# Kernel tuning notes

Measured on AMD Instinct MI355X. Metric: run time of the kernel, lower is better.

The kernel has to match this reference:

```python
import jax, jax.numpy as jnp
import numpy as np

N, E = 50000, 400000          # nodes, edges
T, R = 4, 8                   # node types, relations (edge types)
H, DK = 8, 32                 # heads, head dim
DIN = DOUT = 256              # in/out feature dim (DOUT = H*DK)
SQRT_DK = float(np.sqrt(DK))


def setup_inputs() -> dict:
    key = jax.random.key(0)
    ks = jax.random.split(key, 12)
    f32 = jnp.float32
    return {
        "x": jax.random.normal(ks[0], (N, DIN), f32),
        "node_type": jax.random.randint(ks[1], (N,), 0, T, jnp.int32),
        "src": jax.random.randint(ks[2], (E,), 0, N, jnp.int32),
        "dst": jax.random.randint(ks[3], (E,), 0, N, jnp.int32),
        "etype": jax.random.randint(ks[4], (E,), 0, R, jnp.int32),
        "Wk": jax.random.normal(ks[5], (T, DOUT, DIN), f32) / np.sqrt(DIN).astype(np.float32),
        "bk": jnp.zeros((T, DOUT), f32),
        "Wq": jax.random.normal(ks[6], (T, DOUT, DIN), f32) / np.sqrt(DIN).astype(np.float32),
        "bq": jnp.zeros((T, DOUT), f32),
        "Wv": jax.random.normal(ks[7], (T, DOUT, DIN), f32) / np.sqrt(DIN).astype(np.float32),
        "bv": jnp.zeros((T, DOUT), f32),
        "Wa": jax.random.normal(ks[8], (T, DOUT, DOUT), f32) / np.sqrt(DOUT).astype(np.float32),
        "ba": jnp.zeros((T, DOUT), f32),
        "rel_pri": jnp.ones((R, H), f32),
        "rel_att": jax.random.normal(ks[9], (R, H, DK, DK), f32) / np.sqrt(DK).astype(np.float32),  # ~xavier
        "rel_msg": jax.random.normal(ks[10], (R, H, DK, DK), f32) / np.sqrt(DK).astype(np.float32),
        "skip": jnp.ones((T,), f32),
    }


def _typed_linear(h, W, b, ntype):
    # per-node-type linear: y_n = W[type_n] @ h_n + b[type_n]
    y = jnp.einsum('ni,tdi->ntd', h, W)                      # [N,T,D] (T is small)
    y = jnp.take_along_axis(y, ntype[:, None, None], axis=1)[:, 0]
    return y + b[ntype]


def _hgt_forward(x, node_type, src, dst, etype,
                 Wk, bk, Wq, bq, Wv, bv, Wa, ba,
                 rel_pri, rel_att, rel_msg, skip):
    # typed k/q/v projections -> [N,H,DK]
    K = _typed_linear(x, Wk, bk, node_type).reshape(N, H, DK)
    Q = _typed_linear(x, Wq, bq, node_type).reshape(N, H, DK)
    V = _typed_linear(x, Wv, bv, node_type).reshape(N, H, DK)

    k_e, q_e, v_e = K[src], Q[dst], V[src]                   # [E,H,DK] gathers

    # per-relation head transforms (loop over small fixed R, masked accumulate)
    key_e = jnp.zeros_like(k_e)
    msg_e = jnp.zeros_like(v_e)
    for r in range(R):
        m = (etype == r)[:, None, None].astype(x.dtype)
        key_e = key_e + m * jnp.einsum('ehd,hdf->ehf', k_e, rel_att[r])
        msg_e = msg_e + m * jnp.einsum('ehd,hdf->ehf', v_e, rel_msg[r])

    att = (q_e * key_e).sum(-1) * rel_pri[etype] / SQRT_DK   # [E,H]

    # softmax per (dst node, edge type) segment, then mean across edge types
    seg = dst * R + etype                                    # [E]
    S = N * R
    amax = jax.ops.segment_max(att, seg, num_segments=S)     # [S,H]
    ex = jnp.exp(att - amax[seg])
    denom = jax.ops.segment_sum(ex, seg, num_segments=S)
    w = ex / denom[seg]                                      # normalized attention [E,H]
    h_seg = jax.ops.segment_sum(w[:, :, None] * msg_e, seg, num_segments=S)  # [S,H,DK]
    cnt = jax.ops.segment_sum(jnp.ones((E,), x.dtype), seg, num_segments=S)  # [S]

    h_nr = h_seg.reshape(N, R, DOUT)
    present = (cnt.reshape(N, R) > 0).astype(x.dtype)        # which etypes hit each node
    t = h_nr.sum(1) / jnp.maximum(present.sum(1), 1.0)[:, None]  # cross_reducer='mean'

    trans = _typed_linear(t, Wa, ba, node_type)              # per-type output linear
    alpha = jax.nn.sigmoid(skip)[node_type][:, None]
    return trans * alpha + x * (1.0 - alpha)


def reference(x, node_type, src, dst, etype,
              Wk, bk, Wq, bq, Wv, bv, Wa, ba,
              rel_pri, rel_att, rel_msg, skip):
    return _hgt_forward(x, node_type, src, dst, etype,
                        Wk, bk, Wq, bq, Wv, bv, Wa, ba,
                        rel_pri, rel_att, rel_msg, skip)
```

## Files before the change

### kernel.cpp

```cpp
#include <hip/hip_runtime.h>
#include <math.h>
#include <stdint.h>

#define N_NODES 50000
#define N_EDGES 400000
#define N_T 4
#define N_R 8
#define N_H 8
#define DKD 32
#define D 256
#define TM 64
#define N_SEG (N_NODES * N_R)
#define PROJ_BLOCKS ((N_NODES + TM - 1) / TM + N_T)

typedef __bf16 v8bf __attribute__((ext_vector_type(8)));
typedef float v4f __attribute__((ext_vector_type(4)));
typedef unsigned short u16;

__device__ __forceinline__ u16 f2bf(float f) {
    unsigned int u = __float_as_uint(f);
    u += 0x7fffu + ((u >> 16) & 1u);
    return (u16)(u >> 16);
}

__device__ __forceinline__ void load_bf32(const u16* __restrict__ p, float* f) {
    const uint4* p4 = (const uint4*)p;
    #pragma unroll
    for (int j = 0; j < 4; j++) {
        uint4 u = p4[j];
        f[8 * j + 0] = __uint_as_float(u.x << 16);
        f[8 * j + 1] = __uint_as_float(u.x & 0xffff0000u);
        f[8 * j + 2] = __uint_as_float(u.y << 16);
        f[8 * j + 3] = __uint_as_float(u.y & 0xffff0000u);
        f[8 * j + 4] = __uint_as_float(u.z << 16);
        f[8 * j + 5] = __uint_as_float(u.z & 0xffff0000u);
        f[8 * j + 6] = __uint_as_float(u.w << 16);
        f[8 * j + 7] = __uint_as_float(u.w & 0xffff0000u);
    }
}

__device__ __forceinline__ float dot8f(uint4 m, const float* v) {
    float s;
    s  = __uint_as_float(m.x << 16)          * v[0];
    s += __uint_as_float(m.x & 0xffff0000u)  * v[1];
    s += __uint_as_float(m.y << 16)          * v[2];
    s += __uint_as_float(m.y & 0xffff0000u)  * v[3];
    s += __uint_as_float(m.z << 16)          * v[4];
    s += __uint_as_float(m.z & 0xffff0000u)  * v[5];
    s += __uint_as_float(m.w << 16)          * v[6];
    s += __uint_as_float(m.w & 0xffff0000u)  * v[7];
    return s;
}

__global__ __launch_bounds__(256) void k_cvt4(const float4* __restrict__ s,
                                              ushort4* __restrict__ d, int n4) {
    int i = blockIdx.x * 256 + threadIdx.x;
    if (i < n4) {
        float4 v = s[i];
        ushort4 o;
        o.x = f2bf(v.x); o.y = f2bf(v.y); o.z = f2bf(v.z); o.w = f2bf(v.w);
        d[i] = o;
    }
}

__global__ __launch_bounds__(256) void k_cvt_t(const float* __restrict__ s,
                                               u16* __restrict__ d) {
    int i = blockIdx.x * 256 + threadIdx.x;
    if (i >= N_R * N_H * DKD * DKD) return;
    int mat = i >> 10, w = i & 1023;
    int d0 = w >> 5, f = w & 31;
    d[(mat << 10) + f * DKD + d0] = f2bf(s[i]);
}

__global__ void k_hist(const int* __restrict__ nt, int* __restrict__ cnt) {
    int n = blockIdx.x * blockDim.x + threadIdx.x;
    if (n < N_NODES) atomicAdd(&cnt[nt[n]], 1);
}

__global__ void k_scan(const int* __restrict__ cnt, int* __restrict__ off,
                       int* __restrict__ toff) {
    int o = 0, to = 0;
    for (int t = 0; t < N_T; t++) {
        off[t] = o; toff[t] = to;
        o += cnt[t]; to += (cnt[t] + TM - 1) / TM;
    }
    off[N_T] = o; toff[N_T] = to;
}

__global__ void k_scatter(const int* __restrict__ nt, const int* __restrict__ off,
                          int* __restrict__ cur, int* __restrict__ order) {
    int n = blockIdx.x * blockDim.x + threadIdx.x;
    if (n >= N_NODES) return;
    int t = nt[n];
    int pos = off[t] + atomicAdd(&cur[t], 1);
    order[pos] = n;
}

__global__ void k_hist_seg(const int* __restrict__ dst, const int* __restrict__ et,
                           int* __restrict__ cnt) {
    int e = blockIdx.x * blockDim.x + threadIdx.x;
    if (e < N_EDGES) atomicAdd(&cnt[dst[e] * N_R + et[e]], 1);
}

__global__ __launch_bounds__(1024) void k_scan_l1(const int* __restrict__ cnt,
                                                  int* __restrict__ excl,
                                                  int* __restrict__ bsum) {
    __shared__ int sh[1024];
    int tid = threadIdx.x, i = blockIdx.x * 1024 + tid;
    int v = (i < N_SEG) ? cnt[i] : 0;
    sh[tid] = v;
    __syncthreads();
    #pragma unroll
    for (int ofs = 1; ofs < 1024; ofs <<= 1) {
        int t = (tid >= ofs) ? sh[tid - ofs] : 0;
        __syncthreads();
        sh[tid] += t;
        __syncthreads();
    }
    if (i < N_SEG) excl[i] = sh[tid] - v;
    if (tid == 1023) bsum[blockIdx.x] = sh[1023];
}

__global__ __launch_bounds__(512) void k_scan_l2(int* __restrict__ bsum, int NB) {
    __shared__ int sh[512];
    int tid = threadIdx.x;
    int v = (tid < NB) ? bsum[tid] : 0;
    sh[tid] = v;
    __syncthreads();
    #pragma unroll
    for (int ofs = 1; ofs < 512; ofs <<= 1) {
        int t = (tid >= ofs) ? sh[tid - ofs] : 0;
        __syncthreads();
        sh[tid] += t;
        __syncthreads();
    }
    if (tid < NB) bsum[tid] = sh[tid] - v;
}

__global__ void k_scan_l3(int* __restrict__ excl, const int* __restrict__ bsum) {
    int i = blockIdx.x * blockDim.x + threadIdx.x;
    if (i < N_SEG) excl[i] += bsum[i >> 10];
    else if (i == N_SEG) excl[N_SEG] = N_EDGES;
}

__global__ void k_scatter_seg(const int* __restrict__ src, const int* __restrict__ dst,
                              const int* __restrict__ et, const int* __restrict__ rp,
                              int* __restrict__ cur, int* __restrict__ esrc) {
    int e = blockIdx.x * blockDim.x + threadIdx.x;
    if (e >= N_EDGES) return;
    int sg = dst[e] * N_R + et[e];
    int pos = rp[sg] + atomicAdd(&cur[sg], 1);
    esrc[pos] = src[e];
}

__global__ __launch_bounds__(256) void k_proj(
    const float* __restrict__ x, const int* __restrict__ order,
    const int* __restrict__ off, const int* __restrict__ toff,
    const u16* __restrict__ Wkb, const float* __restrict__ bk,
    const u16* __restrict__ Wqb, const float* __restrict__ bq,
    const u16* __restrict__ Wvb, const float* __restrict__ bv,
    u16* __restrict__ Kb, u16* __restrict__ Qb, u16* __restrict__ Vb) {
    __shared__ __align__(16) u16 xs[TM][D + 8];
    int b = blockIdx.x;
    int t = -1;
    #pragma unroll
    for (int i = 0; i < N_T; i++)
        if (b >= toff[i] && b < toff[i + 1]) t = i;
    if (t < 0) return;
    int nodeBase = off[t] + (b - toff[t]) * TM;
    int count = min(TM, off[t + 1] - nodeBase);
    int tid = threadIdx.x;

    for (int j = tid; j < TM * (D / 4); j += 256) {
        int row = j >> 6, ch = j & 63;
        float4 v = {0.f, 0.f, 0.f, 0.f};
        if (row < count) {
            int g = order[nodeBase + row];
            v = *(const float4*)(x + (size_t)g * D + ch * 4);
        }
        ushort4 o;
        o.x = f2bf(v.x); o.y = f2bf(v.y); o.z = f2bf(v.z); o.w = f2bf(v.w);
        *(ushort4*)&xs[row][ch * 4] = o;
    }
    __syncthreads();

    int lane = tid & 63, wave = tid >> 6;
    int m = lane & 15, quad = lane >> 4;
    v8bf a[8];
    #pragma unroll
    for (int ks = 0; ks < 8; ks++)
        a[ks] = *(const v8bf*)&xs[wave * 16 + m][ks * 32 + quad * 8];

    int grow[4]; bool vrow[4];
    #pragma unroll
    for (int r = 0; r < 4; r++) {
        int rowi = wave * 16 + quad * 4 + r;
        vrow[r] = (rowi < count);
        grow[r] = vrow[r] ? order[nodeBase + rowi] : 0;
    }

    const u16* Ws[3] = {Wkb + (size_t)t * D * D, Wqb + (size_t)t * D * D, Wvb + (size_t)t * D * D};
    const float* Bs[3] = {bk + t * D, bq + t * D, bv + t * D};
    u16* Os[3] = {Kb, Qb, Vb};

    for (int p = 0; p < 3; p++) {
        const u16* W = Ws[p];
        for (int dt = 0; dt < 16; dt++) {
            int dcol = dt * 16 + m;
            v4f acc = {0.f, 0.f, 0.f, 0.f};
            #pragma unroll
            for (int ks = 0; ks < 8; ks++) {
                v8bf bf = *(const v8bf*)(W + (size_t)dcol * D + ks * 32 + quad * 8);
                acc = __builtin_amdgcn_mfma_f32_16x16x32_bf16(a[ks], bf, acc, 0, 0, 0);
            }
            float bias = Bs[p][dcol];
            #pragma unroll
            for (int r = 0; r < 4; r++) {
                if (vrow[r])
                    Os[p][(size_t)grow[r] * D + dcol] = f2bf(acc[r] + bias);
            }
        }
    }
}

__global__ __launch_bounds__(256) void k_fused(
    const u16* __restrict__ Kb, u16* QTb, const u16* __restrict__ Vb,
    const int* __restrict__ rowptr, const int* __restrict__ esrc,
    const u16* __restrict__ Ab, const u16* __restrict__ Mtb,
    const float* __restrict__ pri) {
    __shared__ __align__(16) float Uld[4][N_H][40];
    int wave = threadIdx.x >> 6, lane = threadIdx.x & 63;
    int n = blockIdx.x * 4 + wave;
    if (n >= N_NODES) return;
    int h = lane >> 3, fo = (lane & 7) * 4;
    int base = n * N_R;

    float qv[32];
    load_bf32(QTb + (size_t)n * D + h * DKD, qv);

    float macc[4] = {0.f, 0.f, 0.f, 0.f};
    int np = 0;

    #pragma unroll
    for (int r = 0; r < N_R; r++) {
        int s0 = rowptr[base + r], s1 = rowptr[base + r + 1];
        if (s0 >= s1) continue;
        np++;

        const u16* Ar = Ab + ((size_t)(r * N_H + h) * DKD + fo) * DKD;
        float qtv[4];
        #pragma unroll
        for (int i = 0; i < 4; i++) {
            const uint4* ar = (const uint4*)(Ar + i * DKD);
            qtv[i] = dot8f(ar[0], qv) + dot8f(ar[1], qv + 8)
                   + dot8f(ar[2], qv + 16) + dot8f(ar[3], qv + 24);
        }
        float scale = pri[r * N_H + h] * 0.17677669529663687f;

        float dtmp = 0.f, u0 = 0.f, u1 = 0.f, u2 = 0.f, u3 = 0.f;
        for (int ei = s0; ei < s1; ei++) {
            int s = esrc[ei];
            uint2 ku = *(const uint2*)(Kb + (size_t)s * D + h * DKD + fo);
            uint2 vu = *(const uint2*)(Vb + (size_t)s * D + h * DKD + fo);
            float p = __uint_as_float(ku.x << 16)         * qtv[0]
                    + __uint_as_float(ku.x & 0xffff0000u) * qtv[1]
                    + __uint_as_float(ku.y << 16)         * qtv[2]
                    + __uint_as_float(ku.y & 0xffff0000u) * qtv[3];
            p += __shfl_xor(p, 1);
            p += __shfl_xor(p, 2);
            p += __shfl_xor(p, 4);
            float ex = __expf(p * scale);
            dtmp += ex;
            u0 += ex * __uint_as_float(vu.x << 16);
            u1 += ex * __uint_as_float(vu.x & 0xffff0000u);
            u2 += ex * __uint_as_float(vu.y << 16);
            u3 += ex * __uint_as_float(vu.y & 0xffff0000u);
        }

        float invd = 1.f / dtmp;
        float4 uw = {u0 * invd, u1 * invd, u2 * invd, u3 * invd};
        __builtin_amdgcn_wave_barrier();
        *(float4*)&Uld[wave][h][fo] = uw;
        __builtin_amdgcn_wave_barrier();

        float Uv[32];
        #pragma unroll
        for (int i = 0; i < 8; i++)
            *(float4*)&Uv[4 * i] = *(const float4*)&Uld[wave][h][4 * i];

        const u16* mp = Mtb + ((size_t)(r * N_H + h) * DKD + fo) * DKD;
        #pragma unroll
        for (int j = 0; j < 4; j++) {
            const uint4* mr = (const uint4*)(mp + j * DKD);
            macc[j] += dot8f(mr[0], Uv) + dot8f(mr[1], Uv + 8)
                     + dot8f(mr[2], Uv + 16) + dot8f(mr[3], Uv + 24);
        }
        __builtin_amdgcn_wave_barrier();
    }

    float invp = (np > 0) ? 1.f / (float)np : 1.f;
    ushort4 o;
    o.x = f2bf(macc[0] * invp); o.y = f2bf(macc[1] * invp);
    o.z = f2bf(macc[2] * invp); o.w = f2bf(macc[3] * invp);
    *(ushort4*)(QTb + (size_t)n * D + h * DKD + fo) = o;
}

__global__ __launch_bounds__(256) void k_out(
    const u16* __restrict__ TBF, const float* __restrict__ x,
    const int* __restrict__ order, const int* __restrict__ off, const int* __restrict__ toff,
    const u16* __restrict__ Wab, const float* __restrict__ ba,
    const float* __restrict__ skip, float* __restrict__ out) {
    __shared__ __align__(16) u16 xs[TM][D + 8];
    int b = blockIdx.x;
    int t = -1;
    #pragma unroll
    for (int i = 0; i < N_T; i++)
        if (b >= toff[i] && b < toff[i + 1]) t = i;
    if (t < 0) return;
    int nodeBase = off[t] + (b - toff[t]) * TM;
    int count = min(TM, off[t + 1] - nodeBase);
    int tid = threadIdx.x;

    for (int j = tid; j < TM * 32; j += 256) {
        int row = j >> 5, ch = j & 31;
        ushort4 z = {0, 0, 0, 0};
        if (row < count) {
            int g = order[nodeBase + row];
            const ushort4* p = (const ushort4*)(TBF + (size_t)g * D + ch * 8);
            *(ushort4*)&xs[row][ch * 8] = p[0];
            *(ushort4*)&xs[row][ch * 8 + 4] = p[1];
        } else {
            *(ushort4*)&xs[row][ch * 8] = z;
            *(ushort4*)&xs[row][ch * 8 + 4] = z;
        }
    }
    __syncthreads();

    int lane = tid & 63, wave = tid >> 6;
    int m = lane & 15, quad = lane >> 4;
    v8bf a[8];
    #pragma unroll
    for (int ks = 0; ks < 8; ks++)
        a[ks] = *(const v8bf*)&xs[wave * 16 + m][ks * 32 + quad * 8];

    int grow[4]; bool vrow[4];
    #pragma unroll
    for (int r = 0; r < 4; r++) {
        int rowi = wave * 16 + quad * 4 + r;
        vrow[r] = (rowi < count);
        grow[r] = vrow[r] ? order[nodeBase + rowi] : 0;
    }

    float sv = skip[t];
    float alpha = 1.f / (1.f + __expf(-sv));
    float beta = 1.f - alpha;
    const u16* W = Wab + (size_t)t * D * D;

    for (int dt = 0; dt < 16; dt++) {
        int dcol = dt * 16 + m;
        v4f acc = {0.f, 0.f, 0.f, 0.f};
        #pragma unroll
        for (int ks = 0; ks < 8; ks++) {
            v8bf bf = *(const v8bf*)(W + (size_t)dcol * D + ks * 32 + quad * 8);
            acc = __builtin_amdgcn_mfma_f32_16x16x32_bf16(a[ks], bf, acc, 0, 0, 0);
        }
        float bias = ba[t * D + dcol];
        #pragma unroll
        for (int r = 0; r < 4; r++) {
            if (vrow[r]) {
                size_t o = (size_t)grow[r] * D + dcol;
                out[o] = alpha * (acc[r] + bias) + beta * x[o];
            }
        }
    }
}

extern "C" void kernel_launch(void* const* d_in, const int* in_sizes, int n_in,
                              void* d_out, int out_size, void* d_ws, size_t ws_size,
                              hipStream_t stream) {
    const float* x       = (const float*)d_in[0];
    const int* node_type = (const int*)d_in[1];
    const int* src       = (const int*)d_in[2];
    const int* dst       = (const int*)d_in[3];
    const int* etype     = (const int*)d_in[4];
    const float* Wk = (const float*)d_in[5];
    const float* bk = (const float*)d_in[6];
    const float* Wq = (const float*)d_in[7];
    const float* bq = (const float*)d_in[8];
    const float* Wv = (const float*)d_in[9];
    const float* bv = (const float*)d_in[10];
    const float* Wa = (const float*)d_in[11];
    const float* ba = (const float*)d_in[12];
    const float* rel_pri = (const float*)d_in[13];
    const float* rel_att = (const float*)d_in[14];
    const float* rel_msg = (const float*)d_in[15];
    const float* skip    = (const float*)d_in[16];
    float* out = (float*)d_out;
    char* ws = (char*)d_ws;

    const size_t SZH = (size_t)N_NODES * D * 2;
    const size_t WSZ = (size_t)N_T * D * D;
    const size_t RSZ = (size_t)N_R * N_H * DKD * DKD;
    u16* Kb  = (u16*)(ws);
    u16* Qb  = (u16*)(ws + SZH);
    u16* Vb  = (u16*)(ws + 2 * SZH);
    u16* TBF = Qb;
    u16* Wkb = (u16*)(ws + 3 * SZH);
    u16* Wqb = Wkb + WSZ;
    u16* Wvb = Wqb + WSZ;
    u16* Wab = Wvb + WSZ;
    u16* Ab  = Wab + WSZ;
    u16* Mtb = Ab + RSZ;
    int* order = (int*)(Mtb + RSZ);
    int* small = order + N_NODES;
    int* cnt  = small;
    int* cur  = small + 4;
    int* offp = small + 8;
    int* toffp= small + 13;

    char* ob = (char*)d_out;
    int* rowptr_seg = (int*)ob;
    int* cnt_seg    = rowptr_seg + (N_SEG + 16);
    int* cur_seg    = cnt_seg + N_SEG;
    int* esrc       = cur_seg + N_SEG;
    int* bsum       = esrc + N_EDGES;

    hipMemsetAsync(small, 0, 8 * sizeof(int), stream);
    hipMemsetAsync(cnt_seg, 0, 2 * (size_t)N_SEG * sizeof(int), stream);

    k_cvt4<<<(WSZ / 4 + 255) / 256, 256, 0, stream>>>((const float4*)Wk, (ushort4*)Wkb, WSZ / 4);
    k_cvt4<<<(WSZ / 4 + 255) / 256, 256, 0, stream>>>((const float4*)Wq, (ushort4*)Wqb, WSZ / 4);
    k_cvt4<<<(WSZ / 4 + 255) / 256, 256, 0, stream>>>((const float4*)Wv, (ushort4*)Wvb, WSZ / 4);
    k_cvt4<<<(WSZ / 4 + 255) / 256, 256, 0, stream>>>((const float4*)Wa, (ushort4*)Wab, WSZ / 4);
    k_cvt4<<<(RSZ / 4 + 255) / 256, 256, 0, stream>>>((const float4*)rel_att, (ushort4*)Ab, RSZ / 4);
    k_cvt_t<<<(RSZ + 255) / 256, 256, 0, stream>>>(rel_msg, Mtb);

    k_hist<<<(N_NODES + 255) / 256, 256, 0, stream>>>(node_type, cnt);
    k_scan<<<1, 1, 0, stream>>>(cnt, offp, toffp);
    k_scatter<<<(N_NODES + 255) / 256, 256, 0, stream>>>(node_type, offp, cur, order);

    const int NB = (N_SEG + 1023) / 1024;
    k_hist_seg<<<(N_EDGES + 255) / 256, 256, 0, stream>>>(dst, etype, cnt_seg);
    k_scan_l1<<<NB, 1024, 0, stream>>>(cnt_seg, rowptr_seg, bsum);
    k_scan_l2<<<1, 512, 0, stream>>>(bsum, NB);
    k_scan_l3<<<(N_SEG + 1 + 255) / 256, 256, 0, stream>>>(rowptr_seg, bsum);
    k_scatter_seg<<<(N_EDGES + 255) / 256, 256, 0, stream>>>(src, dst, etype,
                                                             rowptr_seg, cur_seg, esrc);

    k_proj<<<PROJ_BLOCKS, 256, 0, stream>>>(x, order, offp, toffp,
                                            Wkb, bk, Wqb, bq, Wvb, bv, Kb, Qb, Vb);

    k_fused<<<(N_NODES + 3) / 4, 256, 0, stream>>>(Kb, Qb, Vb, rowptr_seg, esrc,
                                                   Ab, Mtb, rel_pri);

    k_out<<<PROJ_BLOCKS, 256, 0, stream>>>(TBF, x, order, offp, toffp,
                                           Wab, ba, skip, out);
}
```

Before: 2.097 ms.

## Flatten per-relation edge loops into one batched loop with packed relation ids

The fused attention kernel now walks all of a node's incoming edges in one flat loop instead of one loop per relation. The relation id is packed into the upper bits of each source index during the scatter. Edge indices are loaded cooperatively 64 at a time and shuffled out, and four edges are processed per iteration so their K/V gathers are in flight together. Per-relation q-transforms, softmax denominators and accumulators are kept in registers and selected through switch statements, so the kernel uses more registers and pays for wave-uniform branching.

```diff
diff --git a/kernel.cpp b/kernel.cpp
--- a/kernel.cpp
+++ b/kernel.cpp
@@ -11,6 +11,7 @@
 #define D 256
 #define TM 64
 #define N_SEG (N_NODES * N_R)
+#define EMASK 0xFFFFF
 #define PROJ_BLOCKS ((N_NODES + TM - 1) / TM + N_T)
 
 typedef __bf16 v8bf __attribute__((ext_vector_type(8)));
@@ -148,9 +149,10 @@
                               int* __restrict__ cur, int* __restrict__ esrc) {
     int e = blockIdx.x * blockDim.x + threadIdx.x;
     if (e >= N_EDGES) return;
-    int sg = dst[e] * N_R + et[e];
+    int r = et[e];
+    int sg = dst[e] * N_R + r;
     int pos = rp[sg] + atomicAdd(&cur[sg], 1);
-    esrc[pos] = src[e];
+    esrc[pos] = src[e] | (r << 20);
 }
 
 __global__ __launch_bounds__(256) void k_proj(
@@ -235,59 +237,122 @@
     int h = lane >> 3, fo = (lane & 7) * 4;
     int base = n * N_R;
 
+    int bnd[N_R + 1];
+    #pragma unroll
+    for (int i = 0; i <= N_R; i++) bnd[i] = rowptr[base + i];
+
     float qv[32];
     load_bf32(QTb + (size_t)n * D + h * DKD, qv);
 
-    float macc[4] = {0.f, 0.f, 0.f, 0.f};
+    float qt[N_R][4];
     int np = 0;
-
     #pragma unroll
     for (int r = 0; r < N_R; r++) {
-        int s0 = rowptr[base + r], s1 = rowptr[base + r + 1];
-        if (s0 >= s1) continue;
+        if (bnd[r] >= bnd[r + 1]) continue;
         np++;
-
         const u16* Ar = Ab + ((size_t)(r * N_H + h) * DKD + fo) * DKD;
-        float qtv[4];
+        float scale = pri[r * N_H + h] * 0.17677669529663687f;
         #pragma unroll
         for (int i = 0; i < 4; i++) {
             const uint4* ar = (const uint4*)(Ar + i * DKD);
-            qtv[i] = dot8f(ar[0], qv) + dot8f(ar[1], qv + 8)
-                   + dot8f(ar[2], qv + 16) + dot8f(ar[3], qv + 24);
-        }
-        float scale = pri[r * N_H + h] * 0.17677669529663687f;
-
-        float dtmp = 0.f, u0 = 0.f, u1 = 0.f, u2 = 0.f, u3 = 0.f;
-        for (int ei = s0; ei < s1; ei++) {
-            int s = esrc[ei];
-            uint2 ku = *(const uint2*)(Kb + (size_t)s * D + h * DKD + fo);
-            uint2 vu = *(const uint2*)(Vb + (size_t)s * D + h * DKD + fo);
-            float p = __uint_as_float(ku.x << 16)         * qtv[0]
-                    + __uint_as_float(ku.x & 0xffff0000u) * qtv[1]
-                    + __uint_as_float(ku.y << 16)         * qtv[2]
-                    + __uint_as_float(ku.y & 0xffff0000u) * qtv[3];
-            p += __shfl_xor(p, 1);
-            p += __shfl_xor(p, 2);
-            p += __shfl_xor(p, 4);
-            float ex = __expf(p * scale);
-            dtmp += ex;
-            u0 += ex * __uint_as_float(vu.x << 16);
-            u1 += ex * __uint_as_float(vu.x & 0xffff0000u);
-            u2 += ex * __uint_as_float(vu.y << 16);
-            u3 += ex * __uint_as_float(vu.y & 0xffff0000u);
-        }
-
-        float invd = 1.f / dtmp;
-        float4 uw = {u0 * invd, u1 * invd, u2 * invd, u3 * invd};
+            qt[r][i] = scale * (dot8f(ar[0], qv) + dot8f(ar[1], qv + 8)
+                     + dot8f(ar[2], qv + 16) + dot8f(ar[3], qv + 24));
+        }
+    }
+
+    float den[N_R] = {0.f, 0.f, 0.f, 0.f, 0.f, 0.f, 0.f, 0.f};
+    float ua[N_R][4] = {};
+
+#define DOTQ(P, RS, KU) { \
+    float _k0 = __uint_as_float((KU).x << 16); \
+    float _k1 = __uint_as_float((KU).x & 0xffff0000u); \
+    float _k2 = __uint_as_float((KU).y << 16); \
+    float _k3 = __uint_as_float((KU).y & 0xffff0000u); \
+    switch (RS) { \
+    case 0: P = _k0*qt[0][0]+_k1*qt[0][1]+_k2*qt[0][2]+_k3*qt[0][3]; break; \
+    case 1: P = _k0*qt[1][0]+_k1*qt[1][1]+_k2*qt[1][2]+_k3*qt[1][3]; break; \
+    case 2: P = _k0*qt[2][0]+_k1*qt[2][1]+_k2*qt[2][2]+_k3*qt[2][3]; break; \
+    case 3: P = _k0*qt[3][0]+_k1*qt[3][1]+_k2*qt[3][2]+_k3*qt[3][3]; break; \
+    case 4: P = _k0*qt[4][0]+_k1*qt[4][1]+_k2*qt[4][2]+_k3*qt[4][3]; break; \
+    case 5: P = _k0*qt[5][0]+_k1*qt[5][1]+_k2*qt[5][2]+_k3*qt[5][3]; break; \
+    case 6: P = _k0*qt[6][0]+_k1*qt[6][1]+_k2*qt[6][2]+_k3*qt[6][3]; break; \
+    default: P = _k0*qt[7][0]+_k1*qt[7][1]+_k2*qt[7][2]+_k3*qt[7][3]; break; } }
+
+#define ACCR(R, EX, V0, V1, V2, V3) \
+    den[R] += EX; ua[R][0] += EX*V0; ua[R][1] += EX*V1; ua[R][2] += EX*V2; ua[R][3] += EX*V3;
+
+#define ACCE(RS, EX, VU) { \
+    float _v0 = __uint_as_float((VU).x << 16); \
+    float _v1 = __uint_as_float((VU).x & 0xffff0000u); \
+    float _v2 = __uint_as_float((VU).y << 16); \
+    float _v3 = __uint_as_float((VU).y & 0xffff0000u); \
+    switch (RS) { \
+    case 0: ACCR(0, EX, _v0, _v1, _v2, _v3) break; \
+    case 1: ACCR(1, EX, _v0, _v1, _v2, _v3) break; \
+    case 2: ACCR(2, EX, _v0, _v1, _v2, _v3) break; \
+    case 3: ACCR(3, EX, _v0, _v1, _v2, _v3) break; \
+    case 4: ACCR(4, EX, _v0, _v1, _v2, _v3) break; \
+    case 5: ACCR(5, EX, _v0, _v1, _v2, _v3) break; \
+    case 6: ACCR(6, EX, _v0, _v1, _v2, _v3) break; \
+    default: ACCR(7, EX, _v0, _v1, _v2, _v3) break; } }
+
+    int eb = bnd[0], ee = bnd[N_R];
+    size_t hoff = (size_t)(h * DKD + fo);
+    for (int w0 = eb; w0 < ee; w0 += 64) {
+        int wcnt = min(64, ee - w0);
+        int myek = (lane < wcnt) ? esrc[w0 + lane] : 0;
+        for (int i0 = 0; i0 < wcnt; i0 += 4) {
+            int mc = wcnt - i0;
+            int pk0 = __shfl(myek, i0);
+            int pk1 = __shfl(myek, i0 + (mc > 1 ? 1 : 0));
+            int pk2 = __shfl(myek, i0 + (mc > 2 ? 2 : 0));
+            int pk3 = __shfl(myek, i0 + (mc > 3 ? 3 : 0));
+            int s0 = pk0 & EMASK, s1 = pk1 & EMASK, s2 = pk2 & EMASK, s3 = pk3 & EMASK;
+            int r0 = __builtin_amdgcn_readfirstlane(pk0) >> 20;
+            int r1 = __builtin_amdgcn_readfirstlane(pk1) >> 20;
+            int r2 = __builtin_amdgcn_readfirstlane(pk2) >> 20;
+            int r3 = __builtin_amdgcn_readfirstlane(pk3) >> 20;
+            uint2 ku0 = *(const uint2*)(Kb + (size_t)s0 * D + hoff);
+            uint2 ku1 = *(const uint2*)(Kb + (size_t)s1 * D + hoff);
+            uint2 ku2 = *(const uint2*)(Kb + (size_t)s2 * D + hoff);
+            uint2 ku3 = *(const uint2*)(Kb + (size_t)s3 * D + hoff);
+            uint2 vu0 = *(const uint2*)(Vb + (size_t)s0 * D + hoff);
+            uint2 vu1 = *(const uint2*)(Vb + (size_t)s1 * D + hoff);
+            uint2 vu2 = *(const uint2*)(Vb + (size_t)s2 * D + hoff);
+            uint2 vu3 = *(const uint2*)(Vb + (size_t)s3 * D + hoff);
+            float p0, p1, p2, p3;
+            DOTQ(p0, r0, ku0);
+            DOTQ(p1, r1, ku1);
+            DOTQ(p2, r2, ku2);
+            DOTQ(p3, r3, ku3);
+            p0 += __shfl_xor(p0, 1); p1 += __shfl_xor(p1, 1);
+            p2 += __shfl_xor(p2, 1); p3 += __shfl_xor(p3, 1);
+            p0 += __shfl_xor(p0, 2); p1 += __shfl_xor(p1, 2);
+            p2 += __shfl_xor(p2, 2); p3 += __shfl_xor(p3, 2);
+            p0 += __shfl_xor(p0, 4); p1 += __shfl_xor(p1, 4);
+            p2 += __shfl_xor(p2, 4); p3 += __shfl_xor(p3, 4);
+            float ex0 = __expf(p0), ex1 = __expf(p1);
+            float ex2 = __expf(p2), ex3 = __expf(p3);
+            ACCE(r0, ex0, vu0);
+            if (mc > 1) { ACCE(r1, ex1, vu1); }
+            if (mc > 2) { ACCE(r2, ex2, vu2); }
+            if (mc > 3) { ACCE(r3, ex3, vu3); }
+        }
+    }
+
+    float macc[4] = {0.f, 0.f, 0.f, 0.f};
+    #pragma unroll
+    for (int r = 0; r < N_R; r++) {
+        if (bnd[r] >= bnd[r + 1]) continue;
+        float invd = 1.f / den[r];
+        float4 uw = {ua[r][0] * invd, ua[r][1] * invd, ua[r][2] * invd, ua[r][3] * invd};
         __builtin_amdgcn_wave_barrier();
         *(float4*)&Uld[wave][h][fo] = uw;
         __builtin_amdgcn_wave_barrier();
-
         float Uv[32];
         #pragma unroll
         for (int i = 0; i < 8; i++)
             *(float4*)&Uv[4 * i] = *(const float4*)&Uld[wave][h][4 * i];
-
         const u16* mp = Mtb + ((size_t)(r * N_H + h) * DKD + fo) * DKD;
         #pragma unroll
         for (int j = 0; j < 4; j++) {
@@ -302,7 +367,7 @@
     ushort4 o;
     o.x = f2bf(macc[0] * invp); o.y = f2bf(macc[1] * invp);
     o.z = f2bf(macc[2] * invp); o.w = f2bf(macc[3] * invp);
-    *(ushort4*)(QTb + (size_t)n * D + h * DKD + fo) = o;
+    *(ushort4*)(QTb + (size_t)n * D + hoff) = o;
 }
 
 __global__ __launch_bounds__(256) void k_out(
```

After: 2.020 ms. 3.7% less time.
